# Performance work log

Hardware: AMD Instinct MI355X
Metric: run time of the kernel (lower is better)

## Reference

```python
import jax, jax.numpy as jnp
import numpy as np

PAD = 4          # displacement radius
WIN = 2 * PAD + 1  # 9 -> 81 displacement channels


def setup_inputs() -> dict:
    key = jax.random.key(0)
    k1, k2 = jax.random.split(key)
    B, C, H, W = 4, 128, 128, 256
    first = jax.random.normal(k1, (B, C, H, W), dtype=jnp.float32)
    second = jax.random.normal(k2, (B, C, H, W), dtype=jnp.float32)
    return {"first": first, "second": second}


def reference(first, second):
    """FlowNet-style correlation / cost volume.

    out[b, (p+4)*9 + (o+4), y, x] = mean_c first[b,c,y,x] * second_pad[b,c,y+p+4,x+o+4]
    with second zero-padded by 4 on each spatial side.
    """
    B, C, H, W = first.shape
    second_pad = jnp.pad(second, ((0, 0), (0, 0), (PAD, PAD), (PAD, PAD)))
    outs = []
    for p in range(WIN):        # vertical displacement index (p - 4)
        for o in range(WIN):    # horizontal displacement index (o - 4)
            shifted = second_pad[:, :, p:p + H, o:o + W]  # [B,C,H,W]
            outs.append(jnp.mean(first * shifted, axis=1))  # [B,H,W]
    return jnp.stack(outs, axis=1)  # [B,81,H,W]
```

## Files before the change

### kernel.cpp

```cpp
#include <hip/hip_runtime.h>
#include <hip/hip_bf16.h>


namespace {
constexpr int kC = 128, kH = 128, kW = 256;
constexpr int kWin = 9;
constexpr int kYB = 4, kXB = 16;
constexpr int kSR = kYB + 8;
constexpr int kSX = kXB + 16;
constexpr int kCP = 40;
constexpr int kKC = 32;
constexpr int kSSz = kSR * kSX * kCP;
constexpr int kFSz = kYB * kXB * kCP;
constexpr int kBuf = kSSz + kFSz;
constexpr int kSU = kSR * (kSX / 4) * (kKC / 8);
constexpr int kFU = kYB * (kXB / 4) * (kKC / 8);
constexpr int kTU = kSU + kFU;
constexpr int kThreads = 512;
constexpr int kBlocks = 4 * (kH / kYB) * (kW / kXB);
constexpr int kOS = kYB * kXB + 4;
constexpr int kCStr = kH * kW;

typedef __attribute__((ext_vector_type(8))) short bf16x8;
typedef __attribute__((ext_vector_type(4))) float f32x4;

__device__ __forceinline__ void bar_lgkm() {
    asm volatile("s_waitcnt lgkmcnt(0)\n\ts_barrier" ::: "memory");
}
}

__global__ __launch_bounds__(kThreads, 4) void corr_mfma(
    const float* __restrict__ first,
    const float* __restrict__ second,
    float* __restrict__ out)
{
    __shared__ __align__(16) unsigned short lds[2 * kBuf];

    const int tid  = threadIdx.x;
    const int lane = tid & 63;
    const int wid  = tid >> 6;
    const int yslot = wid >> 1;
    const int Ns    = wid & 1;

    const int bid = blockIdx.x;
    const int xcd = bid & 7;
    const int seq = bid >> 3;
    const int xt  = seq & 15;
    const int g   = ((seq >> 4) << 3) + xcd;
    const int b   = g >> 5;
    const int y0  = (g & 31) * kYB;
    const int X0  = xt * kXB;

    const size_t ibase = (size_t)b * kC * kCStr;

    const float* ug = nullptr;
    int ul = -1;
    if (tid < kSU) {
        int co = tid & 3, xq = (tid >> 2) & 7, row = tid >> 5;
        int yg = y0 - 4 + row, xg = X0 - 8 + xq * 4;
        ul = (row * kSX + xq * 4) * kCP + co * 8;
        if (yg >= 0 && yg < kH && xg >= 0 && xg <= kW - 4)
            ug = second + ibase + (size_t)(co * 8) * kCStr + (size_t)yg * kW + xg;
    } else if (tid < kTU) {
        int u2 = tid - kSU;
        int co = u2 & 3, xq = (u2 >> 2) & 3, row = u2 >> 4;
        ul = kSSz + (row * kXB + xq * 4) * kCP + co * 8;
        ug = first + ibase + (size_t)(co * 8) * kCStr
                   + (size_t)(y0 + row) * kW + (X0 + xq * 4);
    }

    float4 pvA[8], pvB[8];
    auto issue = [&](float4* pv, int kc) {
        if (ul < 0) return;
        const float4 z = make_float4(0.f, 0.f, 0.f, 0.f);
#pragma unroll
        for (int j = 0; j < 8; ++j) pv[j] = z;
        if (ug) {
            const float* gp = ug + (size_t)kc * kKC * kCStr;
#pragma unroll
            for (int j = 0; j < 8; ++j)
                pv[j] = *(const float4*)(gp + (size_t)j * kCStr);
        }
    };
    auto write_lds = [&](int base, const float4* pv) {
        if (ul < 0) return;
#pragma unroll
        for (int xi = 0; xi < 4; ++xi) {
            union { uint4 q; __hip_bfloat162 h[4]; } pk;
#pragma unroll
            for (int jj = 0; jj < 4; ++jj) {
                float lo = ((const float*)&pv[2 * jj])[xi];
                float hi = ((const float*)&pv[2 * jj + 1])[xi];
                pk.h[jj] = __float22bfloat162_rn(make_float2(lo, hi));
            }
            *(uint4*)&lds[base + ul + xi * kCP] = pk.q;
        }
    };

    const int l15 = lane & 15, lg = lane >> 4;
    const int aoff = kSSz + (yslot * kXB + l15) * kCP + lg * 8;
    const int boff = (yslot * kSX + Ns * 16 + l15) * kCP + lg * 8;

    f32x4 acc[kWin];
    {
        f32x4 z = {0.f, 0.f, 0.f, 0.f};
#pragma unroll
        for (int p = 0; p < kWin; ++p) acc[p] = z;
    }

    auto compute = [&](int base) {
        bf16x8 a = *(const bf16x8*)&lds[base + aoff];
#pragma unroll
        for (int p = 0; p < kWin; ++p) {
            bf16x8 bb = *(const bf16x8*)&lds[base + boff + p * (kSX * kCP)];
            acc[p] = __builtin_amdgcn_mfma_f32_16x16x32_bf16(a, bb, acc[p], 0, 0, 0);
        }
    };

    issue(pvA, 0);
    issue(pvB, 1);
    __builtin_amdgcn_sched_barrier(0);
    write_lds(0, pvA);
    bar_lgkm();
    issue(pvA, 2);
    __builtin_amdgcn_sched_barrier(0);
    compute(0);
    write_lds(kBuf, pvB);
    bar_lgkm();
    issue(pvB, 3);
    __builtin_amdgcn_sched_barrier(0);
    compute(kBuf);
    write_lds(0, pvA);
    bar_lgkm();
    compute(0);
    write_lds(kBuf, pvB);
    bar_lgkm();
    compute(kBuf);

    float* outb = (float*)lds;
    const float inv = 1.0f / (float)kC;
    const int delta = Ns ? 12 : -4;
#pragma unroll
    for (int p = 0; p < kWin; ++p)
#pragma unroll
        for (int r = 0; r < 4; ++r) {
            int m = (lg << 2) + r;
            int o = l15 - m + delta;
            if (o >= 0 && o < kWin) {
                int d = p * kWin + o;
                outb[d * kOS + yslot * kXB + m] = acc[p][r] * inv;
            }
        }
    bar_lgkm();

    const size_t ob = (size_t)b * (kWin * kWin) * kCStr;
    for (int i = tid; i < kWin * kWin * kYB * (kXB / 4); i += kThreads) {
        int d  = i >> 4;
        int r2 = i & 15;
        int yy = r2 >> 2, xq = r2 & 3;
        float4 v = *(const float4*)&outb[d * kOS + yy * kXB + xq * 4];
        *(float4*)&out[ob + ((size_t)d * kH + (y0 + yy)) * kW + X0 + xq * 4] = v;
    }
}

extern "C" void kernel_launch(void* const* d_in, const int* in_sizes, int n_in,
                              void* d_out, int out_size, void* d_ws, size_t ws_size,
                              hipStream_t stream) {
    const float* first  = (const float*)d_in[0];
    const float* second = (const float*)d_in[1];
    float* out = (float*)d_out;
    dim3 grid(kBlocks);
    dim3 block(kThreads);
    hipLaunchKernelGGL(corr_mfma, grid, block, 0, stream, first, second, out);
}
```

Baseline: 65.95 us.

## Enlarge tile to 8 rows with 1024 threads and XOR-swizzled LDS layout

Doubles the output tile height to 8 rows per block and uses 1024 threads. Each `second` halo tile now covers 16 rows for 8 output rows instead of 12 rows for 4, which cuts redundant halo loads. The channel chunk grows to 64, so there are two pipeline stages instead of four. All of `first` is staged at once, and the LDS layout switches from padded strides to XOR swizzling to avoid bank conflicts. The costs are fewer blocks and a larger LDS footprint, which may reduce occupancy, and less overlap of loads with compute.

Result: no change. 64.72 us (-1.9%).

```diff
diff --git a/kernel.cpp b/kernel.cpp
--- a/kernel.cpp
+++ b/kernel.cpp
@@ -5,18 +5,14 @@
 namespace {
 constexpr int kC = 128, kH = 128, kW = 256;
 constexpr int kWin = 9;
-constexpr int kYB = 4, kXB = 16;
-constexpr int kSR = kYB + 8;
-constexpr int kSX = kXB + 16;
-constexpr int kCP = 40;
-constexpr int kKC = 32;
-constexpr int kSSz = kSR * kSX * kCP;
-constexpr int kFSz = kYB * kXB * kCP;
-constexpr int kBuf = kSSz + kFSz;
-constexpr int kSU = kSR * (kSX / 4) * (kKC / 8);
-constexpr int kFU = kYB * (kXB / 4) * (kKC / 8);
-constexpr int kTU = kSU + kFU;
-constexpr int kThreads = 512;
+constexpr int kYB = 8, kXB = 16;
+constexpr int kSR = 16, kSX = 32;
+constexpr int kKC = 64;
+constexpr int kSBuf = kSR * kSX * kKC;
+constexpr int kFBase = 2 * kSBuf;
+constexpr int kFSz = kYB * kXB * kC;
+constexpr int kLdsE = kFBase + kFSz;
+constexpr int kThreads = 1024;
 constexpr int kBlocks = 4 * (kH / kYB) * (kW / kXB);
 constexpr int kOS = kYB * kXB + 4;
 constexpr int kCStr = kH * kW;
@@ -34,7 +30,7 @@
     const float* __restrict__ second,
     float* __restrict__ out)
 {
-    __shared__ __align__(16) unsigned short lds[2 * kBuf];
+    __shared__ __align__(16) unsigned short lds[kLdsE];
 
     const int tid  = threadIdx.x;
     const int lane = tid & 63;
@@ -47,59 +43,91 @@
     const int seq = bid >> 3;
     const int xt  = seq & 15;
     const int g   = ((seq >> 4) << 3) + xcd;
-    const int b   = g >> 5;
-    const int y0  = (g & 31) * kYB;
+    const int b   = g >> 4;
+    const int y0  = (g & 15) * kYB;
     const int X0  = xt * kXB;
 
     const size_t ibase = (size_t)b * kC * kCStr;
 
-    const float* ug = nullptr;
-    int ul = -1;
-    if (tid < kSU) {
-        int co = tid & 3, xq = (tid >> 2) & 7, row = tid >> 5;
-        int yg = y0 - 4 + row, xg = X0 - 8 + xq * 4;
-        ul = (row * kSX + xq * 4) * kCP + co * 8;
-        if (yg >= 0 && yg < kH && xg >= 0 && xg <= kW - 4)
-            ug = second + ibase + (size_t)(co * 8) * kCStr + (size_t)yg * kW + xg;
-    } else if (tid < kTU) {
-        int u2 = tid - kSU;
-        int co = u2 & 3, xq = (u2 >> 2) & 3, row = u2 >> 4;
-        ul = kSSz + (row * kXB + xq * 4) * kCP + co * 8;
-        ug = first + ibase + (size_t)(co * 8) * kCStr
-                   + (size_t)(y0 + row) * kW + (X0 + xq * 4);
-    }
-
-    float4 pvA[8], pvB[8];
-    auto issue = [&](float4* pv, int kc) {
-        if (ul < 0) return;
+    const int srow = tid >> 6, srem = tid & 63;
+    const int sxq = srem >> 3, sco = srem & 7;
+    const int sy = y0 - 4 + srow, sgx = X0 - 8 + sxq * 4;
+    const float* sg = nullptr;
+    if (sy >= 0 && sy < kH && sgx >= 0 && sgx <= kW - 4)
+        sg = second + ibase + (size_t)(sco * 8) * kCStr + (size_t)sy * kW + sgx;
+    int sul[4];
+#pragma unroll
+    for (int xi = 0; xi < 4; ++xi) {
+        int x = sxq * 4 + xi;
+        sul[xi] = ((srow * kSX + x) << 6) + ((sco ^ (x & 7)) << 3);
+    }
+
+    const int frow = tid >> 7, frem = tid & 127;
+    const int fxq = frem >> 5, fq = frem & 31;
+    const float* fg = first + ibase + (size_t)(fq * 4) * kCStr
+                            + (size_t)(y0 + frow) * kW + (X0 + fxq * 4);
+    int ful[4];
+#pragma unroll
+    for (int xi = 0; xi < 4; ++xi) {
+        int x = fxq * 4 + xi;
+        int o = fq >> 1, h = fq & 1;
+        ful[xi] = kFBase + ((frow * kXB + x) << 7) + ((o ^ (x & 15)) << 3) + h * 4;
+    }
+
+    float4 ps[8], pf[4];
+    auto issue_s = [&](int kc) {
         const float4 z = make_float4(0.f, 0.f, 0.f, 0.f);
 #pragma unroll
-        for (int j = 0; j < 8; ++j) pv[j] = z;
-        if (ug) {
-            const float* gp = ug + (size_t)kc * kKC * kCStr;
+        for (int j = 0; j < 8; ++j) ps[j] = z;
+        if (sg) {
+            const float* gp = sg + (size_t)kc * kKC * kCStr;
 #pragma unroll
             for (int j = 0; j < 8; ++j)
-                pv[j] = *(const float4*)(gp + (size_t)j * kCStr);
-        }
-    };
-    auto write_lds = [&](int base, const float4* pv) {
-        if (ul < 0) return;
+                ps[j] = *(const float4*)(gp + (size_t)j * kCStr);
+        }
+    };
+    auto write_s = [&](int base) {
 #pragma unroll
         for (int xi = 0; xi < 4; ++xi) {
             union { uint4 q; __hip_bfloat162 h[4]; } pk;
 #pragma unroll
             for (int jj = 0; jj < 4; ++jj) {
-                float lo = ((const float*)&pv[2 * jj])[xi];
-                float hi = ((const float*)&pv[2 * jj + 1])[xi];
+                float lo = ((const float*)&ps[2 * jj])[xi];
+                float hi = ((const float*)&ps[2 * jj + 1])[xi];
                 pk.h[jj] = __float22bfloat162_rn(make_float2(lo, hi));
             }
-            *(uint4*)&lds[base + ul + xi * kCP] = pk.q;
+            *(uint4*)&lds[base + sul[xi]] = pk.q;
+        }
+    };
+    auto issue_f = [&]() {
+#pragma unroll
+        for (int j = 0; j < 4; ++j)
+            pf[j] = *(const float4*)(fg + (size_t)j * kCStr);
+    };
+    auto write_f = [&]() {
+#pragma unroll
+        for (int xi = 0; xi < 4; ++xi) {
+            union { uint2 q; __hip_bfloat162 h[2]; } pk;
+            pk.h[0] = __float22bfloat162_rn(make_float2(
+                ((const float*)&pf[0])[xi], ((const float*)&pf[1])[xi]));
+            pk.h[1] = __float22bfloat162_rn(make_float2(
+                ((const float*)&pf[2])[xi], ((const float*)&pf[3])[xi]));
+            *(uint2*)&lds[ful[xi]] = pk.q;
         }
     };
 
     const int l15 = lane & 15, lg = lane >> 4;
-    const int aoff = kSSz + (yslot * kXB + l15) * kCP + lg * 8;
-    const int boff = (yslot * kSX + Ns * 16 + l15) * kCP + lg * 8;
+    int afA[2][2];
+#pragma unroll
+    for (int kc = 0; kc < 2; ++kc)
+#pragma unroll
+        for (int kk = 0; kk < 2; ++kk)
+            afA[kc][kk] = kFBase + ((yslot * kXB + l15) << 7)
+                        + (((kc * 8 + kk * 4 + lg) ^ l15) << 3);
+    const int sx = Ns * 16 + l15;
+    const int o0 = (lg ^ (l15 & 7)) << 3;
+    const int o1 = ((4 + lg) ^ (l15 & 7)) << 3;
+    const int bbase = (yslot * kSX + sx) << 6;
 
     f32x4 acc[kWin];
     {
@@ -107,35 +135,32 @@
 #pragma unroll
         for (int p = 0; p < kWin; ++p) acc[p] = z;
     }
-
-    auto compute = [&](int base) {
-        bf16x8 a = *(const bf16x8*)&lds[base + aoff];
+    auto compute = [&](int kc) {
+        const int sb = kc * kSBuf;
+        bf16x8 a0 = *(const bf16x8*)&lds[afA[kc][0]];
+        bf16x8 a1 = *(const bf16x8*)&lds[afA[kc][1]];
 #pragma unroll
         for (int p = 0; p < kWin; ++p) {
-            bf16x8 bb = *(const bf16x8*)&lds[base + boff + p * (kSX * kCP)];
-            acc[p] = __builtin_amdgcn_mfma_f32_16x16x32_bf16(a, bb, acc[p], 0, 0, 0);
-        }
-    };
-
-    issue(pvA, 0);
-    issue(pvB, 1);
+            const int rb = sb + bbase + p * (kSX * kKC);
+            bf16x8 b0 = *(const bf16x8*)&lds[rb + o0];
+            acc[p] = __builtin_amdgcn_mfma_f32_16x16x32_bf16(a0, b0, acc[p], 0, 0, 0);
+            bf16x8 b1 = *(const bf16x8*)&lds[rb + o1];
+            acc[p] = __builtin_amdgcn_mfma_f32_16x16x32_bf16(a1, b1, acc[p], 0, 0, 0);
+        }
+    };
+
+    issue_s(0);
+    issue_f();
     __builtin_amdgcn_sched_barrier(0);
-    write_lds(0, pvA);
-    bar_lgkm();
-    issue(pvA, 2);
+    write_s(0);
+    write_f();
+    issue_s(1);
     __builtin_amdgcn_sched_barrier(0);
-    compute(0);
-    write_lds(kBuf, pvB);
-    bar_lgkm();
-    issue(pvB, 3);
-    __builtin_amdgcn_sched_barrier(0);
-    compute(kBuf);
-    write_lds(0, pvA);
     bar_lgkm();
     compute(0);
-    write_lds(kBuf, pvB);
+    write_s(kSBuf);
     bar_lgkm();
-    compute(kBuf);
+    compute(1);
 
     float* outb = (float*)lds;
     const float inv = 1.0f / (float)kC;
@@ -155,8 +180,8 @@
 
     const size_t ob = (size_t)b * (kWin * kWin) * kCStr;
     for (int i = tid; i < kWin * kWin * kYB * (kXB / 4); i += kThreads) {
-        int d  = i >> 4;
-        int r2 = i & 15;
+        int d  = i >> 5;
+        int r2 = i & 31;
         int yy = r2 >> 2, xq = r2 & 3;
         float4 v = *(const float4*)&outb[d * kOS + yy * kXB + xq * 4];
         *(float4*)&out[ob + ((size_t)d * kH + (y0 + yy)) * kW + X0 + xq * 4] = v;
```
